# Kernel tuning notes

Hardware: AMD Instinct MI355X
Metric: run time of the kernel (lower is better)

Reference implementation:

```python
import jax, jax.numpy as jnp
import numpy as np


def _unfold(x, r):
    # x: [b, ch, h, w] -> [b, ch, k*k, h, w], zero-padded 3x3-style neighborhoods
    b, ch, h, w = x.shape
    k = 2 * r + 1
    xp = jnp.pad(x, ((0, 0), (0, 0), (r, r), (r, r)))
    patches = [xp[:, :, i:i + h, j:j + w] for i in range(k) for j in range(k)]
    return jnp.stack(patches, axis=2)


def setup_inputs() -> dict:
    key = jax.random.key(0)
    ks = jax.random.split(key, 6)
    b, c, h, w = 4, 128, 128, 128
    scale = 1.0 / np.sqrt(c)
    return {
        "feature0": jax.random.normal(ks[0], (b, c, h, w), jnp.float32),
        "flow": jax.random.normal(ks[1], (b, 2, h, w), jnp.float32),
        "q_w": jax.random.normal(ks[2], (c, c), jnp.float32) * scale,
        "q_b": jax.random.normal(ks[3], (c,), jnp.float32) * 0.01,
        "k_w": jax.random.normal(ks[4], (c, c), jnp.float32) * scale,
        "k_b": jax.random.normal(ks[5], (c,), jnp.float32) * 0.01,
        "local_window_attn": 1,
        "local_window_radius": 1,
    }


def reference(feature0, flow, q_w, q_b, k_w, k_b, local_window_attn, local_window_radius):
    b, c, h, w = feature0.shape
    inv_sqrt_c = 1.0 / jnp.sqrt(jnp.asarray(c, feature0.dtype))
    x = feature0.reshape(b, c, h * w).transpose(0, 2, 1)  # [b, hw, c]
    q = x @ q_w.T + q_b  # q_proj
    if local_window_attn:
        r = local_window_radius
        kf = x @ k_w.T + k_b  # k_proj applied to original feature
        kmap = kf.transpose(0, 2, 1).reshape(b, c, h, w)
        kwin = _unfold(kmap, r)      # [b, c, k2, h, w]
        fwin = _unfold(flow, r)      # [b, 2, k2, h, w]
        qmap = q.reshape(b, h, w, c)
        scores = jnp.einsum('bhwc,bckhw->bhwk', qmap, kwin) * inv_sqrt_c
        prob = jax.nn.softmax(scores, axis=-1)
        out = jnp.einsum('bhwk,bfkhw->bfhw', prob, fwin)  # [b, 2, h, w]
        return out
    else:
        # NOTE: faithful to source, key = k_proj(q_proj(x))
        key_ = q @ k_w.T + k_b
        value = flow.reshape(b, flow.shape[1], h * w).transpose(0, 2, 1)  # [b, hw, 2]
        scores = jnp.einsum('bnc,bmc->bnm', q, key_) * inv_sqrt_c
        prob = jax.nn.softmax(scores, axis=-1)
        out = jnp.einsum('bnm,bmf->bnf', prob, value)
        return out.reshape(b, h, w, value.shape[-1]).transpose(0, 3, 1, 2)
```

## Files before the change

kernel.cpp:

```cpp
#include <hip/hip_runtime.h>


#define HW 16384
#define NB 4
#define TOT (NB * HW)

typedef short bf16x8 __attribute__((ext_vector_type(8)));
typedef float f32x4 __attribute__((ext_vector_type(4)));

__device__ __forceinline__ unsigned short f2bf(float f) {
    unsigned u = __float_as_uint(f);
    return (unsigned short)((u + 0x7fffu + ((u >> 16) & 1u)) >> 16);
}
__device__ __forceinline__ float bf2f(unsigned short s) {
    return __uint_as_float(((unsigned)s) << 16);
}

__global__ void prep_kernel(const float* __restrict__ qw, const float* __restrict__ qb,
                            const float* __restrict__ kw, const float* __restrict__ kb,
                            unsigned short* __restrict__ Mh, unsigned short* __restrict__ Ml,
                            float* __restrict__ u, float* __restrict__ v,
                            float* __restrict__ dptr) {
    __shared__ float red[128];
    int bid = blockIdx.x, tid = threadIdx.x;
    if (bid < 128) {
        int ci = bid;
        int cj = tid & 127, half = tid >> 7;
        int co0 = half * 64;
        const float* qcol = qw + ci;
        float acc = 0.f;
#pragma unroll 4
        for (int co = 0; co < 64; ++co)
            acc += qcol[(size_t)(co0 + co) * 128] * kw[(size_t)(co0 + co) * 128 + cj];
        if (half) red[cj] = acc;
        __syncthreads();
        if (!half) {
            float mval = acc + red[cj];
            unsigned short h = f2bf(mval);
            Mh[ci * 128 + cj] = h;
            Ml[ci * 128 + cj] = f2bf(mval - bf2f(h));
        }
    } else {
        int half = tid >> 7, t = tid & 127;
        const float* w  = half ? kw : qw;
        const float* bv = half ? qb : kb;
        float acc = 0.f;
#pragma unroll 4
        for (int co = 0; co < 128; ++co) acc += w[co * 128 + t] * bv[co];
        if (half) v[t] = acc; else u[t] = acc;
        if (!half) red[t] = qb[t] * kb[t];
        __syncthreads();
        if (tid == 0) {
            float dd = 0.f;
            for (int i = 0; i < 128; ++i) dd += red[i];
            *dptr = dd;
        }
    }
}

__global__ __launch_bounds__(256, 2)
void proj_kernel(const float* __restrict__ feat, const unsigned short* __restrict__ MhG,
                 const unsigned short* __restrict__ MlG,
                 const float* __restrict__ u, const float* __restrict__ v,
                 float* __restrict__ y, float* __restrict__ gmap, float* __restrict__ dmap) {
    int tid = threadIdx.x;
    int W = blockIdx.x * 4 + (tid >> 6);
    int lane = tid & 63;
    int cig = W & 3, pxg = W >> 2;
    int ci0 = cig * 32;
    int P0 = pxg * 64;
    int b = P0 >> 14, p0 = P0 & (HW - 1);
    int m = lane & 15, q = lane >> 4;
    const float* xbase = feat + (size_t)b * 128 * HW + p0;

    f32x4 zero = {0.f, 0.f, 0.f, 0.f};
    f32x4 acc[2][4];
#pragma unroll
    for (int t = 0; t < 2; ++t)
#pragma unroll
        for (int s = 0; s < 4; ++s) acc[t][s] = zero;

    float gacc[4] = {0.f, 0.f, 0.f, 0.f};
    float dacc[4] = {0.f, 0.f, 0.f, 0.f};

#pragma unroll
    for (int kc = 0; kc < 4; ++kc) {
        int c0 = kc * 32;
        bf16x8 ah[2], al[2];
#pragma unroll
        for (int t = 0; t < 2; ++t) {
            int roff = (ci0 + t * 16 + m) * 128 + c0 + q * 8;
            ah[t] = *(const bf16x8*)(MhG + roff);
            al[t] = *(const bf16x8*)(MlG + roff);
        }
        float uu[8], vv[8];
        if (cig == 0) {
#pragma unroll
            for (int j = 0; j < 8; ++j) {
                uu[j] = u[c0 + q * 8 + j];
                vv[j] = v[c0 + q * 8 + j];
            }
        }
        bf16x8 bh[4], bl[4];
#pragma unroll
        for (int s = 0; s < 4; ++s) {
            const float* xp = xbase + (size_t)(c0 + q * 8) * HW + s * 16 + m;
            float xv[8];
#pragma unroll
            for (int j = 0; j < 8; ++j) xv[j] = xp[(size_t)j * HW];
            if (cig == 0) {
#pragma unroll
                for (int j = 0; j < 8; ++j) {
                    gacc[s] += uu[j] * xv[j];
                    dacc[s] += vv[j] * xv[j];
                }
            }
#pragma unroll
            for (int j = 0; j < 8; ++j) {
                unsigned short h = f2bf(xv[j]);
                bh[s][j] = (short)h;
                bl[s][j] = (short)f2bf(xv[j] - bf2f(h));
            }
        }
#pragma unroll
        for (int t = 0; t < 2; ++t)
#pragma unroll
            for (int s = 0; s < 4; ++s) {
                acc[t][s] = __builtin_amdgcn_mfma_f32_16x16x32_bf16(ah[t], bh[s], acc[t][s], 0, 0, 0);
                acc[t][s] = __builtin_amdgcn_mfma_f32_16x16x32_bf16(ah[t], bl[s], acc[t][s], 0, 0, 0);
                acc[t][s] = __builtin_amdgcn_mfma_f32_16x16x32_bf16(al[t], bh[s], acc[t][s], 0, 0, 0);
            }
    }

    int rg = lane >> 4, col = lane & 15;
#pragma unroll
    for (int t = 0; t < 2; ++t)
#pragma unroll
        for (int s = 0; s < 4; ++s) {
            float* yp = y + ((size_t)b * 128 + ci0 + t * 16 + rg * 4) * HW + p0 + s * 16 + col;
#pragma unroll
            for (int r = 0; r < 4; ++r) yp[(size_t)r * HW] = acc[t][s][r];
        }

    if (cig == 0) {
#pragma unroll
        for (int s = 0; s < 4; ++s) {
            float gg = gacc[s];
            gg += __shfl_xor(gg, 16);
            gg += __shfl_xor(gg, 32);
            float dd = dacc[s];
            dd += __shfl_xor(dd, 16);
            dd += __shfl_xor(dd, 32);
            if (lane < 16) {
                gmap[P0 + s * 16 + lane] = gg;
                dmap[P0 + s * 16 + lane] = dd;
            }
        }
    }
}

__global__ __launch_bounds__(512, 2)
void attn_fused_kernel(const float* __restrict__ feat, const float* __restrict__ y,
                       const float* __restrict__ gmap, const float* __restrict__ dmap,
                       const float* __restrict__ dptr, const float* __restrict__ flow,
                       float* __restrict__ out) {
    __shared__ float2 lds[4 * 9 * 128];
    int tid = threadIdx.x;
    int cg = tid >> 7;
    int pp = tid & 127;
    int P = blockIdx.x * 256 + pp * 2;
    int b = P >> 14;
    int p = P & (HW - 1);
    const float* xb = feat + ((size_t)b * 128 + cg * 32) * HW + p;
    const float* yb = y + ((size_t)b * 128 + cg * 32) * HW + p;

    float s0[9], s1[9];
#pragma unroll
    for (int k = 0; k < 9; ++k) { s0[k] = 0.f; s1[k] = 0.f; }

#pragma unroll 2
    for (int c = 0; c < 32; ++c) {
        float2 xv = *(const float2*)(xb + (size_t)c * HW);
        const float* yc = yb + (size_t)c * HW;
#pragma unroll
        for (int dy = 0; dy < 3; ++dy) {
            const float* yr = yc + (dy - 1) * 128;
            float2 a  = *(const float2*)(yr - 2);
            float2 bb = *(const float2*)(yr);
            float2 cc = *(const float2*)(yr + 2);
            s0[dy * 3 + 0] += xv.x * a.y;   s1[dy * 3 + 0] += xv.y * bb.x;
            s0[dy * 3 + 1] += xv.x * bb.x;  s1[dy * 3 + 1] += xv.y * bb.y;
            s0[dy * 3 + 2] += xv.x * bb.y;  s1[dy * 3 + 2] += xv.y * cc.x;
        }
    }
#pragma unroll
    for (int k = 0; k < 9; ++k)
        lds[(cg * 9 + k) * 128 + pp] = make_float2(s0[k], s1[k]);
    __syncthreads();

    if (tid < 256) {
        int P2 = blockIdx.x * 256 + tid;
        int b2 = P2 >> 14, p2 = P2 & (HW - 1);
        int row = p2 >> 7, col = p2 & 127;
        const float inv = 0.08838834764831845f;
        float dconst = *dptr;
        float g = gmap[P2];
        const float* lf = (const float*)lds;

        float sc[9];
        float mx = -1e30f;
#pragma unroll
        for (int k = 0; k < 9; ++k) {
            float ssum = lf[(0 * 9 + k) * 256 + tid] + lf[(1 * 9 + k) * 256 + tid]
                       + lf[(2 * 9 + k) * 256 + tid] + lf[(3 * 9 + k) * 256 + tid];
            int dy = k / 3 - 1, dx = (k % 3) - 1;
            bool valid = ((unsigned)(row + dy) < 128u) && ((unsigned)(col + dx) < 128u);
            int Pn = P2 + dy * 128 + dx;
            Pn = max(0, min(TOT - 1, Pn));
            float s = valid ? (ssum + g + dconst + dmap[Pn]) * inv : 0.f;
            sc[k] = s;
            mx = fmaxf(mx, s);
        }
        float e[9], sum = 0.f;
#pragma unroll
        for (int k = 0; k < 9; ++k) { e[k] = __expf(sc[k] - mx); sum += e[k]; }
        float rs = 1.f / sum;

        float o0 = 0.f, o1 = 0.f;
#pragma unroll
        for (int k = 0; k < 9; ++k) {
            int dy = k / 3 - 1, dx = (k % 3) - 1;
            bool valid = ((unsigned)(row + dy) < 128u) && ((unsigned)(col + dx) < 128u);
            float pr = valid ? e[k] * rs : 0.f;
            int fi0 = b2 * 2 * HW + p2 + dy * 128 + dx;
            fi0 = max(0, min(2 * TOT - 1, fi0));
            int fi1 = (b2 * 2 + 1) * HW + p2 + dy * 128 + dx;
            fi1 = max(0, min(2 * TOT - 1, fi1));
            o0 += pr * flow[fi0];
            o1 += pr * flow[fi1];
        }
        out[(size_t)(b2 * 2) * HW + p2] = o0;
        out[(size_t)(b2 * 2 + 1) * HW + p2] = o1;
    }
}

extern "C" void kernel_launch(void* const* d_in, const int* in_sizes, int n_in,
                              void* d_out, int out_size, void* d_ws, size_t ws_size,
                              hipStream_t stream) {
    const float* feat = (const float*)d_in[0];
    const float* flow = (const float*)d_in[1];
    const float* qw = (const float*)d_in[2];
    const float* qb = (const float*)d_in[3];
    const float* kw = (const float*)d_in[4];
    const float* kb = (const float*)d_in[5];

    float* ws = (float*)d_ws;
    float* u = ws;
    float* v = ws + 128;
    float* dptr = ws + 256;
    unsigned short* Mh = (unsigned short*)(ws + 512);
    unsigned short* Ml = (unsigned short*)(ws + 8704);
    float* y = ws + 16896;
    float* dmap = ws + 8405760;
    float* gmap = ws + 8471296;
    float* out = (float*)d_out;

    prep_kernel<<<129, 256, 0, stream>>>(qw, qb, kw, kb, Mh, Ml, u, v, dptr);
    proj_kernel<<<1024, 256, 0, stream>>>(feat, Mh, Ml, u, v, y, gmap, dmap);
    attn_fused_kernel<<<256, 512, 0, stream>>>(feat, y, gmap, dmap, dptr, flow, out);
}
```

Baseline: 130.6 us.

## Fuse projection and local attention into one kernel using transposed M and LDS

The projection and attention kernels are merged into a single per-row kernel. The combined matrix is transposed so each pixel's query-side vector z = M^T x + v is computed with MFMA into swizzled LDS. Scores are then formed by dotting z with the neighbouring raw features read from global memory, which removes the large y intermediate and the gmap/dmap round trips. The cost is 64KB of LDS per block, lower occupancy, and an extra 9x neighbour read of the feature map from global/cache.

```diff
diff --git a/kernel.cpp b/kernel.cpp
--- a/kernel.cpp
+++ b/kernel.cpp
@@ -18,7 +18,7 @@
 
 __global__ void prep_kernel(const float* __restrict__ qw, const float* __restrict__ qb,
                             const float* __restrict__ kw, const float* __restrict__ kb,
-                            unsigned short* __restrict__ Mh, unsigned short* __restrict__ Ml,
+                            unsigned short* __restrict__ MhT, unsigned short* __restrict__ MlT,
                             float* __restrict__ u, float* __restrict__ v,
                             float* __restrict__ dptr) {
     __shared__ float red[128];
@@ -27,18 +27,18 @@
         int ci = bid;
         int cj = tid & 127, half = tid >> 7;
         int co0 = half * 64;
-        const float* qcol = qw + ci;
+        const float* kcol = kw + ci;
         float acc = 0.f;
 #pragma unroll 4
         for (int co = 0; co < 64; ++co)
-            acc += qcol[(size_t)(co0 + co) * 128] * kw[(size_t)(co0 + co) * 128 + cj];
+            acc += kcol[(size_t)(co0 + co) * 128] * qw[(size_t)(co0 + co) * 128 + cj];
         if (half) red[cj] = acc;
         __syncthreads();
         if (!half) {
             float mval = acc + red[cj];
             unsigned short h = f2bf(mval);
-            Mh[ci * 128 + cj] = h;
-            Ml[ci * 128 + cj] = f2bf(mval - bf2f(h));
+            MhT[ci * 128 + cj] = h;
+            MlT[ci * 128 + cj] = f2bf(mval - bf2f(h));
         }
     } else {
         int half = tid >> 7, t = tid & 127;
@@ -58,166 +58,137 @@
     }
 }
 
-__global__ __launch_bounds__(256, 2)
-void proj_kernel(const float* __restrict__ feat, const unsigned short* __restrict__ MhG,
-                 const unsigned short* __restrict__ MlG,
-                 const float* __restrict__ u, const float* __restrict__ v,
-                 float* __restrict__ y, float* __restrict__ gmap, float* __restrict__ dmap) {
+__global__ __launch_bounds__(512, 4)
+void fused_kernel(const float* __restrict__ feat,
+                  const unsigned short* __restrict__ MhT, const unsigned short* __restrict__ MlT,
+                  const float* __restrict__ u, const float* __restrict__ v,
+                  const float* __restrict__ dptr, const float* __restrict__ flow,
+                  float* __restrict__ out) {
+    __shared__ float zbuf[16384];
     int tid = threadIdx.x;
-    int W = blockIdx.x * 4 + (tid >> 6);
-    int lane = tid & 63;
-    int cig = W & 3, pxg = W >> 2;
-    int ci0 = cig * 32;
-    int P0 = pxg * 64;
-    int b = P0 >> 14, p0 = P0 & (HW - 1);
-    int m = lane & 15, q = lane >> 4;
-    const float* xbase = feat + (size_t)b * 128 * HW + p0;
-
-    f32x4 zero = {0.f, 0.f, 0.f, 0.f};
-    f32x4 acc[2][4];
-#pragma unroll
-    for (int t = 0; t < 2; ++t)
-#pragma unroll
-        for (int s = 0; s < 4; ++s) acc[t][s] = zero;
-
-    float gacc[4] = {0.f, 0.f, 0.f, 0.f};
-    float dacc[4] = {0.f, 0.f, 0.f, 0.f};
-
-#pragma unroll
-    for (int kc = 0; kc < 4; ++kc) {
-        int c0 = kc * 32;
-        bf16x8 ah[2], al[2];
-#pragma unroll
-        for (int t = 0; t < 2; ++t) {
-            int roff = (ci0 + t * 16 + m) * 128 + c0 + q * 8;
-            ah[t] = *(const bf16x8*)(MhG + roff);
-            al[t] = *(const bf16x8*)(MlG + roff);
-        }
-        float uu[8], vv[8];
-        if (cig == 0) {
+    int bid = blockIdx.x;
+    int b = bid >> 7, row = bid & 127;
+    int p0 = row * 128;
+
+    {
+        char* lbase = (char*)zbuf;
+#pragma unroll
+        for (int it = 0; it < 4; ++it) {
+            int chunk = it * 512 + tid;
+            int off = chunk * 16;
+            int swz = off ^ (((off >> 8) & 7) << 4);
+            bf16x8 tv = *(const bf16x8*)((const char*)MhT + off);
+            *(bf16x8*)(lbase + swz) = tv;
+            bf16x8 tv2 = *(const bf16x8*)((const char*)MlT + off);
+            *(bf16x8*)(lbase + 32768 + swz) = tv2;
+        }
+    }
+    __syncthreads();
+
+    {
+        int wave = tid >> 6, lane = tid & 63;
+        int m = lane & 15, q = lane >> 4;
+        int wp0 = wave * 16;
+        const float* xbase = feat + (size_t)b * 128 * HW + p0 + wp0;
+        const char* lbase = (const char*)zbuf;
+
+        f32x4 zero = {0.f, 0.f, 0.f, 0.f};
+        f32x4 acc[8];
+#pragma unroll
+        for (int t = 0; t < 8; ++t) acc[t] = zero;
+
+#pragma unroll
+        for (int kc = 0; kc < 4; ++kc) {
+            int c0 = kc * 32;
+            const float* xp = xbase + (size_t)(c0 + q * 8) * HW + m;
+            float xv[8];
+#pragma unroll
+            for (int j = 0; j < 8; ++j) xv[j] = xp[(size_t)j * HW];
+            bf16x8 bh, bl;
 #pragma unroll
             for (int j = 0; j < 8; ++j) {
-                uu[j] = u[c0 + q * 8 + j];
-                vv[j] = v[c0 + q * 8 + j];
-            }
-        }
-        bf16x8 bh[4], bl[4];
-#pragma unroll
-        for (int s = 0; s < 4; ++s) {
-            const float* xp = xbase + (size_t)(c0 + q * 8) * HW + s * 16 + m;
-            float xv[8];
-#pragma unroll
-            for (int j = 0; j < 8; ++j) xv[j] = xp[(size_t)j * HW];
-            if (cig == 0) {
-#pragma unroll
-                for (int j = 0; j < 8; ++j) {
-                    gacc[s] += uu[j] * xv[j];
-                    dacc[s] += vv[j] * xv[j];
-                }
-            }
-#pragma unroll
-            for (int j = 0; j < 8; ++j) {
-                unsigned short h = f2bf(xv[j]);
-                bh[s][j] = (short)h;
-                bl[s][j] = (short)f2bf(xv[j] - bf2f(h));
-            }
-        }
-#pragma unroll
-        for (int t = 0; t < 2; ++t)
-#pragma unroll
-            for (int s = 0; s < 4; ++s) {
-                acc[t][s] = __builtin_amdgcn_mfma_f32_16x16x32_bf16(ah[t], bh[s], acc[t][s], 0, 0, 0);
-                acc[t][s] = __builtin_amdgcn_mfma_f32_16x16x32_bf16(ah[t], bl[s], acc[t][s], 0, 0, 0);
-                acc[t][s] = __builtin_amdgcn_mfma_f32_16x16x32_bf16(al[t], bh[s], acc[t][s], 0, 0, 0);
-            }
-    }
-
-    int rg = lane >> 4, col = lane & 15;
-#pragma unroll
-    for (int t = 0; t < 2; ++t)
-#pragma unroll
-        for (int s = 0; s < 4; ++s) {
-            float* yp = y + ((size_t)b * 128 + ci0 + t * 16 + rg * 4) * HW + p0 + s * 16 + col;
-#pragma unroll
-            for (int r = 0; r < 4; ++r) yp[(size_t)r * HW] = acc[t][s][r];
-        }
-
-    if (cig == 0) {
-#pragma unroll
-        for (int s = 0; s < 4; ++s) {
-            float gg = gacc[s];
-            gg += __shfl_xor(gg, 16);
-            gg += __shfl_xor(gg, 32);
-            float dd = dacc[s];
-            dd += __shfl_xor(dd, 16);
-            dd += __shfl_xor(dd, 32);
-            if (lane < 16) {
-                gmap[P0 + s * 16 + lane] = gg;
-                dmap[P0 + s * 16 + lane] = dd;
-            }
-        }
-    }
-}
-
-__global__ __launch_bounds__(512, 2)
-void attn_fused_kernel(const float* __restrict__ feat, const float* __restrict__ y,
-                       const float* __restrict__ gmap, const float* __restrict__ dmap,
-                       const float* __restrict__ dptr, const float* __restrict__ flow,
-                       float* __restrict__ out) {
-    __shared__ float2 lds[4 * 9 * 128];
-    int tid = threadIdx.x;
-    int cg = tid >> 7;
-    int pp = tid & 127;
-    int P = blockIdx.x * 256 + pp * 2;
-    int b = P >> 14;
-    int p = P & (HW - 1);
-    const float* xb = feat + ((size_t)b * 128 + cg * 32) * HW + p;
-    const float* yb = y + ((size_t)b * 128 + cg * 32) * HW + p;
-
-    float s0[9], s1[9];
-#pragma unroll
-    for (int k = 0; k < 9; ++k) { s0[k] = 0.f; s1[k] = 0.f; }
-
+                unsigned short hh = f2bf(xv[j]);
+                bh[j] = (short)hh;
+                bl[j] = (short)f2bf(xv[j] - bf2f(hh));
+            }
+            int colb = (c0 + q * 8) * 2;
+            int swzx = ((m & 7) << 4);
+#pragma unroll
+            for (int t = 0; t < 8; ++t) {
+                int offr = ((t * 16 + m) * 256 + colb) ^ swzx;
+                bf16x8 ah = *(const bf16x8*)(lbase + offr);
+                bf16x8 al = *(const bf16x8*)(lbase + 32768 + offr);
+                acc[t] = __builtin_amdgcn_mfma_f32_16x16x32_bf16(ah, bh, acc[t], 0, 0, 0);
+                acc[t] = __builtin_amdgcn_mfma_f32_16x16x32_bf16(ah, bl, acc[t], 0, 0, 0);
+                acc[t] = __builtin_amdgcn_mfma_f32_16x16x32_bf16(al, bh, acc[t], 0, 0, 0);
+            }
+        }
+        __syncthreads();
+        int px = wp0 + (lane & 15);
+        int rg = lane >> 4;
+#pragma unroll
+        for (int t = 0; t < 8; ++t)
+#pragma unroll
+            for (int r = 0; r < 4; ++r) {
+                int c = t * 16 + rg * 4 + r;
+                zbuf[px * 128 + ((c + px) & 127)] = acc[t][r] + v[c];
+            }
+    }
+    __syncthreads();
+
+    {
+        int spx = tid & 127, h = tid >> 7;
+        int p = p0 + spx;
+        float sc[9];
+#pragma unroll
+        for (int k = 0; k < 9; ++k) sc[k] = 0.f;
+        float g = 0.f;
 #pragma unroll 2
-    for (int c = 0; c < 32; ++c) {
-        float2 xv = *(const float2*)(xb + (size_t)c * HW);
-        const float* yc = yb + (size_t)c * HW;
-#pragma unroll
-        for (int dy = 0; dy < 3; ++dy) {
-            const float* yr = yc + (dy - 1) * 128;
-            float2 a  = *(const float2*)(yr - 2);
-            float2 bb = *(const float2*)(yr);
-            float2 cc = *(const float2*)(yr + 2);
-            s0[dy * 3 + 0] += xv.x * a.y;   s1[dy * 3 + 0] += xv.y * bb.x;
-            s0[dy * 3 + 1] += xv.x * bb.x;  s1[dy * 3 + 1] += xv.y * bb.y;
-            s0[dy * 3 + 2] += xv.x * bb.y;  s1[dy * 3 + 2] += xv.y * cc.x;
-        }
-    }
-#pragma unroll
-    for (int k = 0; k < 9; ++k)
-        lds[(cg * 9 + k) * 128 + pp] = make_float2(s0[k], s1[k]);
+        for (int cc = 0; cc < 32; ++cc) {
+            int c = h * 32 + cc;
+            float zv = zbuf[spx * 128 + ((c + spx) & 127)];
+            const float* xc = feat + ((size_t)b * 128 + c) * HW;
+            float xcen = 0.f;
+#pragma unroll
+            for (int dy = 0; dy < 3; ++dy) {
+                int off = p + (dy - 1) * 128;
+                int om = max(0, min(HW - 1, off - 1));
+                int oc = max(0, min(HW - 1, off));
+                int op = max(0, min(HW - 1, off + 1));
+                float xm = xc[om], x0 = xc[oc], xp1 = xc[op];
+                sc[dy * 3 + 0] += zv * xm;
+                sc[dy * 3 + 1] += zv * x0;
+                sc[dy * 3 + 2] += zv * xp1;
+                if (dy == 1) xcen = x0;
+            }
+            g += u[c] * xcen;
+        }
+        __syncthreads();
+#pragma unroll
+        for (int k = 0; k < 9; ++k)
+            zbuf[(k * 128 + spx) * 4 + h] = sc[k];
+        zbuf[(9 * 128 + spx) * 4 + h] = g;
+    }
     __syncthreads();
 
-    if (tid < 256) {
-        int P2 = blockIdx.x * 256 + tid;
-        int b2 = P2 >> 14, p2 = P2 & (HW - 1);
-        int row = p2 >> 7, col = p2 & 127;
+    if (tid < 128) {
+        int spx = tid;
+        int p = p0 + spx;
+        int col = spx;
         const float inv = 0.08838834764831845f;
         float dconst = *dptr;
-        float g = gmap[P2];
-        const float* lf = (const float*)lds;
+        float g = zbuf[(9 * 128 + spx) * 4 + 0] + zbuf[(9 * 128 + spx) * 4 + 1]
+                + zbuf[(9 * 128 + spx) * 4 + 2] + zbuf[(9 * 128 + spx) * 4 + 3];
 
         float sc[9];
         float mx = -1e30f;
 #pragma unroll
         for (int k = 0; k < 9; ++k) {
-            float ssum = lf[(0 * 9 + k) * 256 + tid] + lf[(1 * 9 + k) * 256 + tid]
-                       + lf[(2 * 9 + k) * 256 + tid] + lf[(3 * 9 + k) * 256 + tid];
             int dy = k / 3 - 1, dx = (k % 3) - 1;
+            float ssum = zbuf[(k * 128 + spx) * 4 + 0] + zbuf[(k * 128 + spx) * 4 + 1]
+                       + zbuf[(k * 128 + spx) * 4 + 2] + zbuf[(k * 128 + spx) * 4 + 3];
             bool valid = ((unsigned)(row + dy) < 128u) && ((unsigned)(col + dx) < 128u);
-            int Pn = P2 + dy * 128 + dx;
-            Pn = max(0, min(TOT - 1, Pn));
-            float s = valid ? (ssum + g + dconst + dmap[Pn]) * inv : 0.f;
+            float s = valid ? (ssum + g + dconst) * inv : 0.f;
             sc[k] = s;
             mx = fmaxf(mx, s);
         }
@@ -232,15 +203,13 @@
             int dy = k / 3 - 1, dx = (k % 3) - 1;
             bool valid = ((unsigned)(row + dy) < 128u) && ((unsigned)(col + dx) < 128u);
             float pr = valid ? e[k] * rs : 0.f;
-            int fi0 = b2 * 2 * HW + p2 + dy * 128 + dx;
-            fi0 = max(0, min(2 * TOT - 1, fi0));
-            int fi1 = (b2 * 2 + 1) * HW + p2 + dy * 128 + dx;
-            fi1 = max(0, min(2 * TOT - 1, fi1));
-            o0 += pr * flow[fi0];
-            o1 += pr * flow[fi1];
-        }
-        out[(size_t)(b2 * 2) * HW + p2] = o0;
-        out[(size_t)(b2 * 2 + 1) * HW + p2] = o1;
+            int poff = p + dy * 128 + dx;
+            poff = max(0, min(HW - 1, poff));
+            o0 += pr * flow[(size_t)(b * 2) * HW + poff];
+            o1 += pr * flow[(size_t)(b * 2 + 1) * HW + poff];
+        }
+        out[(size_t)(b * 2) * HW + p] = o0;
+        out[(size_t)(b * 2 + 1) * HW + p] = o1;
     }
 }
 
@@ -258,14 +227,10 @@
     float* u = ws;
     float* v = ws + 128;
     float* dptr = ws + 256;
-    unsigned short* Mh = (unsigned short*)(ws + 512);
-    unsigned short* Ml = (unsigned short*)(ws + 8704);
-    float* y = ws + 16896;
-    float* dmap = ws + 8405760;
-    float* gmap = ws + 8471296;
+    unsigned short* MhT = (unsigned short*)(ws + 512);
+    unsigned short* MlT = (unsigned short*)(ws + 8704);
     float* out = (float*)d_out;
 
-    prep_kernel<<<129, 256, 0, stream>>>(qw, qb, kw, kb, Mh, Ml, u, v, dptr);
-    proj_kernel<<<1024, 256, 0, stream>>>(feat, Mh, Ml, u, v, y, gmap, dmap);
-    attn_fused_kernel<<<256, 512, 0, stream>>>(feat, y, gmap, dmap, dptr, flow, out);
-}
+    prep_kernel<<<129, 256, 0, stream>>>(qw, qb, kw, kb, MhT, MlT, u, v, dptr);
+    fused_kernel<<<512, 512, 0, stream>>>(feat, MhT, MlT, u, v, dptr, flow, out);
+}
```

After: 116.6 us. 10.7% less time.
